# Optimization experiments

Hardware: AMD Instinct MI355X
Metric: run time of the kernel (lower is better)

The kernel has to match this reference:

```python
import jax, jax.numpy as jnp
import numpy as np

N, D, K = 65536, 512, 5


def setup_inputs() -> dict:
    key = jax.random.key(0)
    k0, k1, k2, k3, k4 = jax.random.split(key, 5)
    x = jax.random.normal(k0, (N, D), dtype=jnp.float32)
    is_protected = jax.random.randint(k1, (N,), 0, 2) > 0  # bool mask
    alpha_p = jax.random.uniform(k2, (D,), dtype=jnp.float32, minval=0.9, maxval=1.1)
    classif_w = jax.random.normal(k3, (K, 1), dtype=jnp.float32)
    centroids = jax.random.normal(k4, (K, D), dtype=jnp.float32)
    return {"x": x, "is_protected": is_protected, "alpha_p": alpha_p,
            "classif_w": classif_w, "centroids": centroids}


def reference(x, is_protected, alpha_p, classif_w, centroids):
    # NOTE: original torch forward applies alpha_p to both the protected and
    # non-protected rows (alpha_np is unused), so the mask split is a no-op
    # and we compute the mapping over all rows at once.
    # distances: sum_d alpha_d * (x_nd - c_kd)^2  -> (n, k)
    diff2 = (x[:, None, :] - centroids[None, :, :]) ** 2  # (n, k, d)
    dist = jnp.einsum("nkd,d->nk", diff2, alpha_p)
    mapping = jax.nn.softmax(dist, axis=-1)              # (n, k)
    reconstructed = mapping @ centroids                  # (n, d)
    pred = (mapping @ jax.nn.sigmoid(classif_w)).ravel() # (n,)
    return mapping, reconstructed, pred
```

## Files before the change

### kernel.cpp

```cpp
#include <hip/hip_runtime.h>
#include <math.h>

#define LFR_N 65536
#define LFR_D 512
#define LFR_K 5
#define ROWS   4
#define BLOCKS 1024
#define NWAVES (BLOCKS * 4)
#define ITERS  (LFR_N / (NWAVES * ROWS))

__global__ __launch_bounds__(256) void lfr_kernel(
    const float* __restrict__ x,
    const float* __restrict__ alpha,
    const float* __restrict__ w,
    const float* __restrict__ cent,
    float* __restrict__ out_map,
    float* __restrict__ out_rec,
    float* __restrict__ out_pred)
{
    const int lane = threadIdx.x & 63;
    const int wib  = threadIdx.x >> 6;
    const int wid  = blockIdx.x * (blockDim.x >> 6) + wib;

    const int dA  = lane * 4;
    const int hi  = (lane >> 5) & 1;
    const int mid = (lane >> 4) & 1;

    float al[8];
    {
        float4 a0 = *(const float4*)(alpha + dA);
        float4 a1 = *(const float4*)(alpha + dA + 256);
        al[0]=a0.x; al[1]=a0.y; al[2]=a0.z; al[3]=a0.w;
        al[4]=a1.x; al[5]=a1.y; al[6]=a1.z; al[7]=a1.w;
    }
    float c[LFR_K][8];
    #pragma unroll
    for (int k = 0; k < LFR_K; ++k) {
        float4 c0 = *(const float4*)(cent + k * LFR_D + dA);
        float4 c1 = *(const float4*)(cent + k * LFR_D + dA + 256);
        c[k][0]=c0.x; c[k][1]=c0.y; c[k][2]=c0.z; c[k][3]=c0.w;
        c[k][4]=c1.x; c[k][5]=c1.y; c[k][6]=c1.z; c[k][7]=c1.w;
    }
    float m2a[8];
    #pragma unroll
    for (int j = 0; j < 8; ++j) m2a[j] = -2.0f * al[j];
    float cst[LFR_K];
    #pragma unroll
    for (int k = 0; k < LFR_K; ++k) {
        float s = 0.0f;
        #pragma unroll
        for (int j = 0; j < 8; ++j) {
            float u = al[j] * c[k][j];
            s = fmaf(u, c[k][j], s);
        }
        cst[k] = s;
    }
    float sigw[LFR_K];
    #pragma unroll
    for (int k = 0; k < LFR_K; ++k)
        sigw[k] = 1.0f / (1.0f + __expf(-w[k]));

    const size_t XSTEP = (size_t)NWAVES * ROWS * LFR_D;
    const float* xp = x + (size_t)wid * ROWS * LFR_D;

    float4 xl[ROWS][2];
    #pragma unroll
    for (int r = 0; r < ROWS; ++r) {
        xl[r][0] = *(const float4*)(xp + (size_t)r * LFR_D + dA);
        xl[r][1] = *(const float4*)(xp + (size_t)r * LFR_D + dA + 256);
    }

    for (int it = 0; it < ITERS; ++it) {
        const size_t rbase = (size_t)(it * NWAVES + wid) * ROWS;

        float p[ROWS][LFR_K];
        #pragma unroll
        for (int r = 0; r < ROWS; ++r) {
            float v[8];
            v[0]=m2a[0]*xl[r][0].x; v[1]=m2a[1]*xl[r][0].y;
            v[2]=m2a[2]*xl[r][0].z; v[3]=m2a[3]*xl[r][0].w;
            v[4]=m2a[4]*xl[r][1].x; v[5]=m2a[5]*xl[r][1].y;
            v[6]=m2a[6]*xl[r][1].z; v[7]=m2a[7]*xl[r][1].w;
            #pragma unroll
            for (int k = 0; k < LFR_K; ++k) {
                float acc = cst[k];
                #pragma unroll
                for (int j = 0; j < 8; ++j) acc = fmaf(c[k][j], v[j], acc);
                p[r][k] = acc;
            }
            if (it + 1 < ITERS) {
                const float* nx = xp + XSTEP + (size_t)r * LFR_D;
                xl[r][0] = *(const float4*)(nx + dA);
                xl[r][1] = *(const float4*)(nx + dA + 256);
            }
        }

        float q[2][LFR_K];
        #pragma unroll
        for (int r2 = 0; r2 < 2; ++r2) {
            #pragma unroll
            for (int k = 0; k < LFR_K; ++k) {
                float send = hi ? p[r2][k]     : p[2 + r2][k];
                float keep = hi ? p[2 + r2][k] : p[r2][k];
                q[r2][k] = keep + __shfl_xor(send, 32);
            }
        }
        float s[LFR_K];
        #pragma unroll
        for (int k = 0; k < LFR_K; ++k) {
            float send = mid ? q[0][k] : q[1][k];
            float keep = mid ? q[1][k] : q[0][k];
            s[k] = keep + __shfl_xor(send, 16);
        }
        #pragma unroll
        for (int off = 8; off > 0; off >>= 1) {
            #pragma unroll
            for (int k = 0; k < LFR_K; ++k)
                s[k] += __shfl_xor(s[k], off);
        }

        float e[LFR_K];
        {
            float mx = s[0];
            #pragma unroll
            for (int k = 1; k < LFR_K; ++k) mx = fmaxf(mx, s[k]);
            float sum = 0.0f;
            #pragma unroll
            for (int k = 0; k < LFR_K; ++k) { e[k] = __expf(s[k] - mx); sum += e[k]; }
            float inv = 1.0f / sum;
            #pragma unroll
            for (int k = 0; k < LFR_K; ++k) e[k] *= inv;
        }

        if ((lane & 15) == 0) {
            const int g = lane >> 4;
            float* mp = out_map + (rbase + g) * LFR_K;
            *(float4*)(mp) = make_float4(e[0], e[1], e[2], e[3]);
            mp[4] = e[4];
            float pr = e[0] * sigw[0];
            #pragma unroll
            for (int k = 1; k < LFR_K; ++k) pr = fmaf(e[k], sigw[k], pr);
            out_pred[rbase + g] = pr;
        }

        float mA[2][LFR_K];
        #pragma unroll
        for (int k = 0; k < LFR_K; ++k) {
            float o = __shfl_xor(e[k], 16);
            mA[0][k] = mid ? o    : e[k];
            mA[1][k] = mid ? e[k] : o;
        }
        float M[ROWS][LFR_K];
        #pragma unroll
        for (int r2 = 0; r2 < 2; ++r2) {
            #pragma unroll
            for (int k = 0; k < LFR_K; ++k) {
                float o = __shfl_xor(mA[r2][k], 32);
                M[r2][k]     = hi ? o         : mA[r2][k];
                M[2 + r2][k] = hi ? mA[r2][k] : o;
            }
        }

        #pragma unroll
        for (int r = 0; r < ROWS; ++r) {
            float rv[8];
            #pragma unroll
            for (int j = 0; j < 8; ++j) {
                float acc = M[r][0] * c[0][j];
                #pragma unroll
                for (int k = 1; k < LFR_K; ++k) acc = fmaf(M[r][k], c[k][j], acc);
                rv[j] = acc;
            }
            float* rr = out_rec + (rbase + r) * LFR_D;
            *(float4*)(rr + dA)       = make_float4(rv[0], rv[1], rv[2], rv[3]);
            *(float4*)(rr + dA + 256) = make_float4(rv[4], rv[5], rv[6], rv[7]);
        }

        xp += XSTEP;
    }
}

extern "C" void kernel_launch(void* const* d_in, const int* in_sizes, int n_in,
                              void* d_out, int out_size, void* d_ws, size_t ws_size,
                              hipStream_t stream) {
    const float* x     = (const float*)d_in[0];
    const float* alpha = (const float*)d_in[2];
    const float* w     = (const float*)d_in[3];
    const float* cent  = (const float*)d_in[4];

    float* out   = (float*)d_out;
    float* o_map = out;
    float* o_rec = out + (size_t)LFR_N * LFR_K;
    float* o_prd = out + (size_t)LFR_N * LFR_K + (size_t)LFR_N * LFR_D;

    dim3 grid(BLOCKS), block(256);
    lfr_kernel<<<grid, block, 0, stream>>>(x, alpha, w, cent, o_map, o_rec, o_prd);
}
```

Baseline: 244.9 us.

## Split fused kernel into separate mapping and reconstruction kernels, double grid size

The single fused kernel is split in two. The first kernel reads x and computes the softmax mapping and pred. The second kernel reads the mapping back from global memory and writes the reconstruction from centroids held in registers. The grid also grows from 1024 to 2048 blocks. The intent is to separate the read-heavy and write-heavy phases so each kernel can stream at full bandwidth. The cost is an extra launch and a small extra round trip of the mapping through global memory.

```diff
diff --git a/kernel.cpp b/kernel.cpp
--- a/kernel.cpp
+++ b/kernel.cpp
@@ -4,18 +4,18 @@
 #define LFR_N 65536
 #define LFR_D 512
 #define LFR_K 5
-#define ROWS   4
-#define BLOCKS 1024
-#define NWAVES (BLOCKS * 4)
-#define ITERS  (LFR_N / (NWAVES * ROWS))
-
-__global__ __launch_bounds__(256) void lfr_kernel(
+#define ROWS    4
+#define BLOCKS  2048
+#define NWAVES  (BLOCKS * 4)
+#define ITERS   (LFR_N / (NWAVES * ROWS))
+
+
+__global__ __launch_bounds__(256) void lfr_map_kernel(
     const float* __restrict__ x,
     const float* __restrict__ alpha,
     const float* __restrict__ w,
     const float* __restrict__ cent,
     float* __restrict__ out_map,
-    float* __restrict__ out_rec,
     float* __restrict__ out_pred)
 {
     const int lane = threadIdx.x & 63;
@@ -131,7 +131,6 @@
             #pragma unroll
             for (int k = 0; k < LFR_K; ++k) e[k] *= inv;
         }
-
         if ((lane & 15) == 0) {
             const int g = lane >> 4;
             float* mp = out_map + (rbase + g) * LFR_K;
@@ -143,23 +142,39 @@
             out_pred[rbase + g] = pr;
         }
 
-        float mA[2][LFR_K];
-        #pragma unroll
-        for (int k = 0; k < LFR_K; ++k) {
-            float o = __shfl_xor(e[k], 16);
-            mA[0][k] = mid ? o    : e[k];
-            mA[1][k] = mid ? e[k] : o;
-        }
+        xp += XSTEP;
+    }
+}
+
+__global__ __launch_bounds__(256) void lfr_rec_kernel(
+    const float* __restrict__ cent,
+    const float* __restrict__ map,
+    float* __restrict__ out_rec)
+{
+    const int lane = threadIdx.x & 63;
+    const int wib  = threadIdx.x >> 6;
+    const int wid  = blockIdx.x * (blockDim.x >> 6) + wib;
+    const int dA   = lane * 4;
+
+    float c[LFR_K][8];
+    #pragma unroll
+    for (int k = 0; k < LFR_K; ++k) {
+        float4 c0 = *(const float4*)(cent + k * LFR_D + dA);
+        float4 c1 = *(const float4*)(cent + k * LFR_D + dA + 256);
+        c[k][0]=c0.x; c[k][1]=c0.y; c[k][2]=c0.z; c[k][3]=c0.w;
+        c[k][4]=c1.x; c[k][5]=c1.y; c[k][6]=c1.z; c[k][7]=c1.w;
+    }
+
+    for (int it = 0; it < ITERS; ++it) {
+        const size_t rbase = (size_t)(it * NWAVES + wid) * ROWS;
+
+        const float* mp = map + rbase * LFR_K;
         float M[ROWS][LFR_K];
         #pragma unroll
-        for (int r2 = 0; r2 < 2; ++r2) {
-            #pragma unroll
-            for (int k = 0; k < LFR_K; ++k) {
-                float o = __shfl_xor(mA[r2][k], 32);
-                M[r2][k]     = hi ? o         : mA[r2][k];
-                M[2 + r2][k] = hi ? mA[r2][k] : o;
-            }
-        }
+        for (int r = 0; r < ROWS; ++r)
+            #pragma unroll
+            for (int k = 0; k < LFR_K; ++k)
+                M[r][k] = mp[r * LFR_K + k];
 
         #pragma unroll
         for (int r = 0; r < ROWS; ++r) {
@@ -175,8 +190,6 @@
             *(float4*)(rr + dA)       = make_float4(rv[0], rv[1], rv[2], rv[3]);
             *(float4*)(rr + dA + 256) = make_float4(rv[4], rv[5], rv[6], rv[7]);
         }
-
-        xp += XSTEP;
     }
 }
 
@@ -194,5 +207,6 @@
     float* o_prd = out + (size_t)LFR_N * LFR_K + (size_t)LFR_N * LFR_D;
 
     dim3 grid(BLOCKS), block(256);
-    lfr_kernel<<<grid, block, 0, stream>>>(x, alpha, w, cent, o_map, o_rec, o_prd);
+    lfr_map_kernel<<<grid, block, 0, stream>>>(x, alpha, w, cent, o_map, o_prd);
+    lfr_rec_kernel<<<grid, block, 0, stream>>>(cent, o_map, o_rec);
 }
```

Measured after the change: 246.7 us. About the same (+0.7%).
